# Performance work log

Hardware: AMD Instinct MI355X
Metric: run time of the kernel (lower is better)

## Reference

```python
import jax, jax.numpy as jnp
import numpy as np
from jax import lax

B, T = 64, 512
VOCAB, EMBED, UNITS = 32000, 256, 512


def setup_inputs() -> dict:
    key = jax.random.key(0)
    ks = jax.random.split(key, 8)
    s = 0.05
    G = 4 * UNITS
    return {
        "encoder_input": jax.random.randint(ks[0], (B, T), 0, VOCAB, dtype=jnp.int32),
        "embedding": jax.random.normal(ks[1], (VOCAB, EMBED), jnp.float32) * s,
        "W_fwd": jax.random.normal(ks[2], (EMBED, G), jnp.float32) * s,
        "U_fwd": jax.random.normal(ks[3], (UNITS, G), jnp.float32) * s,
        "b_fwd": jnp.zeros((G,), jnp.float32),
        "W_bwd": jax.random.normal(ks[4], (EMBED, G), jnp.float32) * s,
        "U_bwd": jax.random.normal(ks[5], (UNITS, G), jnp.float32) * s,
        "b_bwd": jnp.zeros((G,), jnp.float32),
    }


def _lstm_scan(x, mask, W, Uw, b, reverse):
    """Masked LSTM over time. Keras semantics: at masked steps the (h, c)
    state is carried through unchanged and the emitted output repeats the
    previous hidden state (which for LSTM equals the carried h).
    x: [B, T, E] float, mask: [B, T] bool."""
    Bsz = x.shape[0]
    Uh = Uw.shape[0]
    # Precompute input projection for all timesteps: [B, T, 4U]
    xz = jnp.einsum("bte,eg->btg", x, W) + b

    def step(carry, inp):
        h, c = carry
        z_x, m = inp  # z_x: [B, 4U], m: [B]
        z = z_x + h @ Uw
        i, f, g, o = jnp.split(z, 4, axis=-1)  # Keras gate order i, f, c, o
        i = jax.nn.sigmoid(i)
        f = jax.nn.sigmoid(f)
        g = jnp.tanh(g)
        o = jax.nn.sigmoid(o)
        c_new = f * c + i * g
        h_new = o * jnp.tanh(c_new)
        m = m[:, None]
        h = jnp.where(m, h_new, h)
        c = jnp.where(m, c_new, c)
        return (h, c), h

    h0 = jnp.zeros((Bsz, Uh), x.dtype)
    c0 = jnp.zeros((Bsz, Uh), x.dtype)
    (h, c), ys = lax.scan(
        step, (h0, c0), (xz.swapaxes(0, 1), mask.T), reverse=reverse
    )
    # lax.scan with reverse=True stacks outputs in original time order,
    # matching Keras Bidirectional's reverse-then-re-reverse behavior.
    return ys.swapaxes(0, 1), h, c


def reference(encoder_input, embedding, W_fwd, U_fwd, b_fwd, W_bwd, U_bwd, b_bwd):
    mask = encoder_input != 0  # mask_zero=True
    emb = embedding[encoder_input]  # [B, T, E]
    out_f, h_f, c_f = _lstm_scan(emb, mask, W_fwd, U_fwd, b_fwd, reverse=False)
    out_b, h_b, c_b = _lstm_scan(emb, mask, W_bwd, U_bwd, b_bwd, reverse=True)
    encoder_output = jnp.concatenate([out_f, out_b], axis=-1)  # [B, T, 2U]
    final_state_h = jnp.concatenate([h_f, h_b], axis=-1)  # [B, 2U]
    final_state_c = jnp.concatenate([c_f, c_b], axis=-1)  # [B, 2U]
    # Dropout is identity at inference (training=False default).
    return encoder_output, final_state_h, final_state_c
```

## Files before the change

### kernel.cpp

```cpp
#include <hip/hip_runtime.h>
#include <cstdint>


#define B_ 64
#define T_ 512
#define E_ 256

typedef __attribute__((ext_vector_type(8))) short bf16x8;
typedef __attribute__((ext_vector_type(4))) float f32x4;

__device__ __forceinline__ unsigned short f2bf(float x) {
  unsigned u = __float_as_uint(x);
  u += 0x7FFFu + ((u >> 16) & 1u);
  return (unsigned short)(u >> 16);
}
__device__ __forceinline__ float sigm(float x) { return 1.0f / (1.0f + __expf(-x)); }
__device__ __forceinline__ float tanh_(float x) { return 1.0f - 2.0f / (__expf(2.0f * x) + 1.0f); }

__global__ void prep_kernel(const int* __restrict__ enc, const float* __restrict__ emb,
                            unsigned short* __restrict__ o) {
  const int bi = blockIdx.x;
  const int t = bi >> 6, b = bi & 63;
  const int tok = enc[b * T_ + t];
  float4 v = ((const float4*)(emb + (size_t)tok * E_))[threadIdx.x];
  ushort4 w;
  w.x = f2bf(v.x); w.y = f2bf(v.y); w.z = f2bf(v.z); w.w = f2bf(v.w);
  ((ushort4*)(o + (size_t)t * (B_ * E_) + b * E_))[threadIdx.x] = w;
}

__global__ __launch_bounds__(256, 1)
void lstm_kernel(const int* __restrict__ enc, const unsigned short* __restrict__ embq,
                 const float* __restrict__ Wf, const float* __restrict__ Uf, const float* __restrict__ bfv,
                 const float* __restrict__ Wb, const float* __restrict__ Ub, const float* __restrict__ bbv,
                 unsigned short* __restrict__ Hbuf, unsigned* __restrict__ cnt,
                 float* __restrict__ out) {
  const int tid = threadIdx.x;
  const int lane = tid & 63;
  const int wave = tid >> 6;
  const int mh = wave & 1, nh = wave >> 1;
  const int l15 = lane & 15, l4 = lane >> 4;
  const int d = blockIdx.x >> 5;
  const int cg = blockIdx.x & 31;
  const int u0 = cg * 16;
  const float* Wd = d ? Wb : Wf;
  const float* Ud = d ? Ub : Uf;
  const float* bd = d ? bbv : bfv;

  __shared__ float Z[64][68];

  bf16x8 u_frag[16][2];
#pragma unroll
  for (int ks = 0; ks < 16; ++ks) {
#pragma unroll
    for (int ns = 0; ns < 2; ++ns) {
      const int gate = nh * 2 + ns;
      const int col = gate * 512 + u0 + l15;
      const int k0 = ks * 32 + l4 * 8;
      bf16x8 f;
#pragma unroll
      for (int i = 0; i < 8; ++i) f[i] = (short)f2bf(Ud[(size_t)(k0 + i) * 2048 + col]);
      u_frag[ks][ns] = f;
    }
  }
  bf16x8 w_frag[8][2];
#pragma unroll
  for (int ks = 0; ks < 8; ++ks) {
#pragma unroll
    for (int ns = 0; ns < 2; ++ns) {
      const int gate = nh * 2 + ns;
      const int col = gate * 512 + u0 + l15;
      const int k0 = ks * 32 + l4 * 8;
      bf16x8 f;
#pragma unroll
      for (int i = 0; i < 8; ++i) f[i] = (short)f2bf(Wd[(size_t)(k0 + i) * 2048 + col]);
      w_frag[ks][ns] = f;
    }
  }

  const int ej = tid & 15;
  const int ebg = tid >> 4;
  float bias[4];
#pragma unroll
  for (int g = 0; g < 4; ++g) bias[g] = bd[g * 512 + u0 + ej];

  float hst[4] = {0.f, 0.f, 0.f, 0.f}, cst[4] = {0.f, 0.f, 0.f, 0.f};

  bf16x8 apf[8][2];
  int mpf[4];
  {
    const int t0 = d ? 511 : 0;
    const unsigned short* eT = embq + (size_t)t0 * (B_ * E_);
#pragma unroll
    for (int ks = 0; ks < 8; ++ks)
#pragma unroll
      for (int ms = 0; ms < 2; ++ms) {
        const int b = mh * 32 + ms * 16 + l15;
        const int e0 = ks * 32 + l4 * 8;
        apf[ks][ms] = *(const bf16x8*)(eT + b * E_ + e0);
      }
#pragma unroll
    for (int r = 0; r < 4; ++r) mpf[r] = enc[(ebg * 4 + r) * T_ + t0];
  }

  unsigned* cntd = cnt + d * 513;

  for (int s = 0; s < 512; ++s) {
    const int t = d ? (511 - s) : s;
    f32x4 acc[2][2];
#pragma unroll
    for (int ms = 0; ms < 2; ++ms)
#pragma unroll
      for (int ns = 0; ns < 2; ++ns) acc[ms][ns] = (f32x4)0.0f;

#pragma unroll
    for (int ks = 0; ks < 8; ++ks)
#pragma unroll
      for (int ms = 0; ms < 2; ++ms)
#pragma unroll
        for (int ns = 0; ns < 2; ++ns)
          acc[ms][ns] = __builtin_amdgcn_mfma_f32_16x16x32_bf16(apf[ks][ms], w_frag[ks][ns],
                                                                acc[ms][ns], 0, 0, 0);

    if (s > 0) {
      if (tid == 0) {
        while (__hip_atomic_load(cntd + s, __ATOMIC_RELAXED, __HIP_MEMORY_SCOPE_AGENT) < 32u) {}
      }
      __syncthreads();

      bf16x8 ha[16][2];
      {
        const unsigned short* Hrd = Hbuf + ((size_t)((s & 1) * 2 + d)) * 32768;
        const char* lb = (const char*)Hrd + (l4 >> 1) * 2048 + mh * 1024 + l15 * 32 + (l4 & 1) * 16;
        const char* b0p = lb + 0 * 8192 + 4096;
        const char* b1p = lb + 1 * 8192 + 4096;
        const char* b2p = lb + 2 * 8192 + 4096;
        const char* b3p = lb + 3 * 8192 + 4096;
        const char* b4p = lb + 4 * 8192 + 4096;
        const char* b5p = lb + 5 * 8192 + 4096;
        const char* b6p = lb + 6 * 8192 + 4096;
        const char* b7p = lb + 7 * 8192 + 4096;
        asm volatile(
          "global_load_dwordx4 %0, %32, off offset:-4096 sc0 sc1\n\t"
          "global_load_dwordx4 %1, %32, off offset:-3584 sc0 sc1\n\t"
          "global_load_dwordx4 %2, %32, off offset:0 sc0 sc1\n\t"
          "global_load_dwordx4 %3, %32, off offset:512 sc0 sc1\n\t"
          "global_load_dwordx4 %4, %33, off offset:-4096 sc0 sc1\n\t"
          "global_load_dwordx4 %5, %33, off offset:-3584 sc0 sc1\n\t"
          "global_load_dwordx4 %6, %33, off offset:0 sc0 sc1\n\t"
          "global_load_dwordx4 %7, %33, off offset:512 sc0 sc1\n\t"
          "global_load_dwordx4 %8, %34, off offset:-4096 sc0 sc1\n\t"
          "global_load_dwordx4 %9, %34, off offset:-3584 sc0 sc1\n\t"
          "global_load_dwordx4 %10, %34, off offset:0 sc0 sc1\n\t"
          "global_load_dwordx4 %11, %34, off offset:512 sc0 sc1\n\t"
          "global_load_dwordx4 %12, %35, off offset:-4096 sc0 sc1\n\t"
          "global_load_dwordx4 %13, %35, off offset:-3584 sc0 sc1\n\t"
          "global_load_dwordx4 %14, %35, off offset:0 sc0 sc1\n\t"
          "global_load_dwordx4 %15, %35, off offset:512 sc0 sc1\n\t"
          "global_load_dwordx4 %16, %36, off offset:-4096 sc0 sc1\n\t"
          "global_load_dwordx4 %17, %36, off offset:-3584 sc0 sc1\n\t"
          "global_load_dwordx4 %18, %36, off offset:0 sc0 sc1\n\t"
          "global_load_dwordx4 %19, %36, off offset:512 sc0 sc1\n\t"
          "global_load_dwordx4 %20, %37, off offset:-4096 sc0 sc1\n\t"
          "global_load_dwordx4 %21, %37, off offset:-3584 sc0 sc1\n\t"
          "global_load_dwordx4 %22, %37, off offset:0 sc0 sc1\n\t"
          "global_load_dwordx4 %23, %37, off offset:512 sc0 sc1\n\t"
          "global_load_dwordx4 %24, %38, off offset:-4096 sc0 sc1\n\t"
          "global_load_dwordx4 %25, %38, off offset:-3584 sc0 sc1\n\t"
          "global_load_dwordx4 %26, %38, off offset:0 sc0 sc1\n\t"
          "global_load_dwordx4 %27, %38, off offset:512 sc0 sc1\n\t"
          "global_load_dwordx4 %28, %39, off offset:-4096 sc0 sc1\n\t"
          "global_load_dwordx4 %29, %39, off offset:-3584 sc0 sc1\n\t"
          "global_load_dwordx4 %30, %39, off offset:0 sc0 sc1\n\t"
          "global_load_dwordx4 %31, %39, off offset:512 sc0 sc1\n\t"
          "s_waitcnt vmcnt(0)"
          : "=v"(ha[0][0]), "=v"(ha[0][1]), "=v"(ha[1][0]), "=v"(ha[1][1]),
            "=v"(ha[2][0]), "=v"(ha[2][1]), "=v"(ha[3][0]), "=v"(ha[3][1]),
            "=v"(ha[4][0]), "=v"(ha[4][1]), "=v"(ha[5][0]), "=v"(ha[5][1]),
            "=v"(ha[6][0]), "=v"(ha[6][1]), "=v"(ha[7][0]), "=v"(ha[7][1]),
            "=v"(ha[8][0]), "=v"(ha[8][1]), "=v"(ha[9][0]), "=v"(ha[9][1]),
            "=v"(ha[10][0]), "=v"(ha[10][1]), "=v"(ha[11][0]), "=v"(ha[11][1]),
            "=v"(ha[12][0]), "=v"(ha[12][1]), "=v"(ha[13][0]), "=v"(ha[13][1]),
            "=v"(ha[14][0]), "=v"(ha[14][1]), "=v"(ha[15][0]), "=v"(ha[15][1])
          : "v"(b0p), "v"(b1p), "v"(b2p), "v"(b3p),
            "v"(b4p), "v"(b5p), "v"(b6p), "v"(b7p)
          : "memory");
      }
#pragma unroll
      for (int ks = 0; ks < 16; ++ks) {
        acc[0][0] = __builtin_amdgcn_mfma_f32_16x16x32_bf16(ha[ks][0], u_frag[ks][0], acc[0][0], 0, 0, 0);
        acc[0][1] = __builtin_amdgcn_mfma_f32_16x16x32_bf16(ha[ks][0], u_frag[ks][1], acc[0][1], 0, 0, 0);
        acc[1][0] = __builtin_amdgcn_mfma_f32_16x16x32_bf16(ha[ks][1], u_frag[ks][0], acc[1][0], 0, 0, 0);
        acc[1][1] = __builtin_amdgcn_mfma_f32_16x16x32_bf16(ha[ks][1], u_frag[ks][1], acc[1][1], 0, 0, 0);
      }
    } else {
      __syncthreads();
    }

#pragma unroll
    for (int ms = 0; ms < 2; ++ms)
#pragma unroll
      for (int ns = 0; ns < 2; ++ns)
#pragma unroll
        for (int r = 0; r < 4; ++r)
          Z[mh * 32 + ms * 16 + l4 * 4 + r][nh * 32 + ns * 16 + l15] = acc[ms][ns][r];
    __syncthreads();

    unsigned hu[4];
    {
      const bool last = (s == 511);
#pragma unroll
      for (int r = 0; r < 4; ++r) {
        const int b = ebg * 4 + r;
        float zi = Z[b][ej] + bias[0];
        float zf = Z[b][16 + ej] + bias[1];
        float zg = Z[b][32 + ej] + bias[2];
        float zo = Z[b][48 + ej] + bias[3];
        float ig = sigm(zi), fg = sigm(zf), gg = tanh_(zg), og = sigm(zo);
        float cn = fg * cst[r] + ig * gg;
        float hn = og * tanh_(cn);
        const bool m = (mpf[r] != 0);
        cst[r] = m ? cn : cst[r];
        hst[r] = m ? hn : hst[r];
        hu[r] = (unsigned)f2bf(hst[r]);
        out[((size_t)b * T_ + t) * 1024 + d * 512 + u0 + ej] = hst[r];
        if (last) {
          out[33554432u + (size_t)b * 1024 + d * 512 + u0 + ej] = hst[r];
          out[33619968u + (size_t)b * 1024 + d * 512 + u0 + ej] = cst[r];
        }
      }
    }

    if (s < 511) {
      const int tn = d ? (510 - s) : (s + 1);
      const unsigned short* eT = embq + (size_t)tn * (B_ * E_);
#pragma unroll
      for (int ks = 0; ks < 8; ++ks)
#pragma unroll
        for (int ms = 0; ms < 2; ++ms) {
          const int b = mh * 32 + ms * 16 + l15;
          const int e0 = ks * 32 + l4 * 8;
          apf[ks][ms] = *(const bf16x8*)(eT + b * E_ + e0);
        }
#pragma unroll
      for (int r = 0; r < 4; ++r) mpf[r] = enc[(ebg * 4 + r) * T_ + tn];
    }

    {
      unsigned short* Hwr = Hbuf + ((size_t)(((s + 1) & 1) * 2 + d)) * 32768 + cg * 1024;
      char* hp = (char*)(Hwr + ebg * 64 + ej);
      asm volatile(
        "global_store_short %0, %1, off sc0 sc1\n\t"
        "global_store_short %0, %2, off offset:32 sc0 sc1\n\t"
        "global_store_short %0, %3, off offset:64 sc0 sc1\n\t"
        "global_store_short %0, %4, off offset:96 sc0 sc1\n\t"
        "s_waitcnt vmcnt(0)"
        :: "v"(hp), "v"(hu[0]), "v"(hu[1]), "v"(hu[2]), "v"(hu[3])
        : "memory");
    }
    __syncthreads();
    if (tid == 0)
      __hip_atomic_fetch_add(cntd + (s + 1), 1u, __ATOMIC_RELAXED, __HIP_MEMORY_SCOPE_AGENT);
  }
}

extern "C" void kernel_launch(void* const* d_in, const int* in_sizes, int n_in,
                              void* d_out, int out_size, void* d_ws, size_t ws_size,
                              hipStream_t stream) {
  const int* enc = (const int*)d_in[0];
  const float* emb = (const float*)d_in[1];
  const float* Wf = (const float*)d_in[2];
  const float* Uf = (const float*)d_in[3];
  const float* bf = (const float*)d_in[4];
  const float* Wb = (const float*)d_in[5];
  const float* Ub = (const float*)d_in[6];
  const float* bb = (const float*)d_in[7];
  float* out = (float*)d_out;
  char* ws = (char*)d_ws;

  unsigned short* embq = (unsigned short*)ws;
  unsigned short* Hbuf = (unsigned short*)(ws + (16u << 20));
  unsigned* cnt = (unsigned*)(ws + (16u << 20) + 262144u);

  hipMemsetAsync(ws + (16u << 20) + 262144u, 0, 4104u, stream);
  prep_kernel<<<32768, 64, 0, stream>>>(enc, emb, embq);
  lstm_kernel<<<64, 256, 0, stream>>>(enc, embq, Wf, Uf, bf, Wb, Ub, bb, Hbuf, cnt, out);
}
```

Measured before the change: 3.415 ms.

## Replace persistent spin-synced LSTM kernel with per-timestep kernel launches

```diff
diff --git a/kernel.cpp b/kernel.cpp
--- a/kernel.cpp
+++ b/kernel.cpp
@@ -28,12 +28,37 @@
   ((ushort4*)(o + (size_t)t * (B_ * E_) + b * E_))[threadIdx.x] = w;
 }
 
+__global__ void prep_w(const float* __restrict__ Wf, const float* __restrict__ Uf,
+                       const float* __restrict__ Wb, const float* __restrict__ Ub,
+                       unsigned short* __restrict__ Uq, unsigned short* __restrict__ Wq) {
+  int bi = blockIdx.x;
+  const int ns = bi & 1; bi >>= 1;
+  const int kk = bi % 24; bi /= 24;
+  const int nh = bi & 1; bi >>= 1;
+  const int cg = bi & 31; bi >>= 5;
+  const int d = bi;
+  const int lane = threadIdx.x;
+  const int l15 = lane & 15, l4 = lane >> 4;
+  const bool isU = (kk < 16);
+  const float* src = isU ? (d ? Ub : Uf) : (d ? Wb : Wf);
+  const int ks = isU ? kk : (kk - 16);
+  const int col = (nh * 2 + ns) * 512 + cg * 16 + l15;
+  const int row0 = ks * 32 + l4 * 8;
+  bf16x8 f;
+#pragma unroll
+  for (int i = 0; i < 8; ++i) f[i] = (short)f2bf(src[(size_t)(row0 + i) * 2048 + col]);
+  unsigned short* dst = isU
+    ? Uq + ((size_t)(((d * 32 + cg) * 2 + nh) * 16 + ks) * 2 + ns) * 512 + lane * 8
+    : Wq + ((size_t)(((d * 32 + cg) * 2 + nh) * 8 + ks) * 2 + ns) * 512 + lane * 8;
+  *(bf16x8*)dst = f;
+}
+
 __global__ __launch_bounds__(256, 1)
-void lstm_kernel(const int* __restrict__ enc, const unsigned short* __restrict__ embq,
-                 const float* __restrict__ Wf, const float* __restrict__ Uf, const float* __restrict__ bfv,
-                 const float* __restrict__ Wb, const float* __restrict__ Ub, const float* __restrict__ bbv,
-                 unsigned short* __restrict__ Hbuf, unsigned* __restrict__ cnt,
-                 float* __restrict__ out) {
+void lstm_step(const int s, const int* __restrict__ enc, const unsigned short* __restrict__ embq,
+               const unsigned short* __restrict__ Uq, const unsigned short* __restrict__ Wq,
+               const float* __restrict__ bfv, const float* __restrict__ bbv,
+               unsigned short* __restrict__ Hbf, float* __restrict__ Hf32,
+               float* __restrict__ Cst, float* __restrict__ out) {
   const int tid = threadIdx.x;
   const int lane = tid & 63;
   const int wave = tid >> 6;
@@ -42,224 +67,117 @@
   const int d = blockIdx.x >> 5;
   const int cg = blockIdx.x & 31;
   const int u0 = cg * 16;
-  const float* Wd = d ? Wb : Wf;
-  const float* Ud = d ? Ub : Uf;
-  const float* bd = d ? bbv : bfv;
+  const int t = d ? (T_ - 1 - s) : s;
 
   __shared__ float Z[64][68];
 
+  const unsigned short* ub = Uq + ((size_t)((d * 32 + cg) * 2 + nh)) * (16 * 2 * 512);
+  const unsigned short* wb = Wq + ((size_t)((d * 32 + cg) * 2 + nh)) * (8 * 2 * 512);
   bf16x8 u_frag[16][2];
 #pragma unroll
-  for (int ks = 0; ks < 16; ++ks) {
-#pragma unroll
-    for (int ns = 0; ns < 2; ++ns) {
-      const int gate = nh * 2 + ns;
-      const int col = gate * 512 + u0 + l15;
-      const int k0 = ks * 32 + l4 * 8;
-      bf16x8 f;
-#pragma unroll
-      for (int i = 0; i < 8; ++i) f[i] = (short)f2bf(Ud[(size_t)(k0 + i) * 2048 + col]);
-      u_frag[ks][ns] = f;
+  for (int ks = 0; ks < 16; ++ks)
+#pragma unroll
+    for (int ns = 0; ns < 2; ++ns)
+      u_frag[ks][ns] = *(const bf16x8*)(ub + (size_t)(ks * 2 + ns) * 512 + lane * 8);
+  bf16x8 w_frag[8][2];
+#pragma unroll
+  for (int ks = 0; ks < 8; ++ks)
+#pragma unroll
+    for (int ns = 0; ns < 2; ++ns)
+      w_frag[ks][ns] = *(const bf16x8*)(wb + (size_t)(ks * 2 + ns) * 512 + lane * 8);
+
+  bf16x8 apf[8][2];
+  {
+    const unsigned short* eT = embq + (size_t)t * (B_ * E_);
+#pragma unroll
+    for (int ks = 0; ks < 8; ++ks)
+#pragma unroll
+      for (int ms = 0; ms < 2; ++ms) {
+        const int b = mh * 32 + ms * 16 + l15;
+        apf[ks][ms] = *(const bf16x8*)(eT + b * E_ + ks * 32 + l4 * 8);
+      }
+  }
+  const int ej = tid & 15;
+  const int ebg = tid >> 4;
+  int mpf[4];
+#pragma unroll
+  for (int r = 0; r < 4; ++r) mpf[r] = enc[(ebg * 4 + r) * T_ + t];
+
+  f32x4 acc[2][2];
+#pragma unroll
+  for (int ms = 0; ms < 2; ++ms)
+#pragma unroll
+    for (int ns = 0; ns < 2; ++ns) acc[ms][ns] = (f32x4)0.0f;
+
+#pragma unroll
+  for (int ks = 0; ks < 8; ++ks)
+#pragma unroll
+    for (int ms = 0; ms < 2; ++ms)
+#pragma unroll
+      for (int ns = 0; ns < 2; ++ns)
+        acc[ms][ns] = __builtin_amdgcn_mfma_f32_16x16x32_bf16(apf[ks][ms], w_frag[ks][ns],
+                                                              acc[ms][ns], 0, 0, 0);
+
+  if (s > 0) {
+    const unsigned short* Hrd = Hbf + ((size_t)((s & 1) * 2 + d)) * (B_ * 512);
+    bf16x8 ha[16][2];
+#pragma unroll
+    for (int ks = 0; ks < 16; ++ks)
+#pragma unroll
+      for (int ms = 0; ms < 2; ++ms) {
+        const int b = mh * 32 + ms * 16 + l15;
+        ha[ks][ms] = *(const bf16x8*)(Hrd + (size_t)b * 512 + ks * 32 + l4 * 8);
+      }
+#pragma unroll
+    for (int ks = 0; ks < 16; ++ks) {
+      acc[0][0] = __builtin_amdgcn_mfma_f32_16x16x32_bf16(ha[ks][0], u_frag[ks][0], acc[0][0], 0, 0, 0);
+      acc[0][1] = __builtin_amdgcn_mfma_f32_16x16x32_bf16(ha[ks][0], u_frag[ks][1], acc[0][1], 0, 0, 0);
+      acc[1][0] = __builtin_amdgcn_mfma_f32_16x16x32_bf16(ha[ks][1], u_frag[ks][0], acc[1][0], 0, 0, 0);
+      acc[1][1] = __builtin_amdgcn_mfma_f32_16x16x32_bf16(ha[ks][1], u_frag[ks][1], acc[1][1], 0, 0, 0);
     }
   }
-  bf16x8 w_frag[8][2];
-#pragma unroll
-  for (int ks = 0; ks < 8; ++ks) {
-#pragma unroll
-    for (int ns = 0; ns < 2; ++ns) {
-      const int gate = nh * 2 + ns;
-      const int col = gate * 512 + u0 + l15;
-      const int k0 = ks * 32 + l4 * 8;
-      bf16x8 f;
-#pragma unroll
-      for (int i = 0; i < 8; ++i) f[i] = (short)f2bf(Wd[(size_t)(k0 + i) * 2048 + col]);
-      w_frag[ks][ns] = f;
+
+#pragma unroll
+  for (int ms = 0; ms < 2; ++ms)
+#pragma unroll
+    for (int ns = 0; ns < 2; ++ns)
+#pragma unroll
+      for (int r = 0; r < 4; ++r)
+        Z[mh * 32 + ms * 16 + l4 * 4 + r][nh * 32 + ns * 16 + l15] = acc[ms][ns][r];
+  __syncthreads();
+
+  const float* bd = d ? bbv : bfv;
+  float bias[4];
+#pragma unroll
+  for (int g = 0; g < 4; ++g) bias[g] = bd[g * 512 + u0 + ej];
+
+  float* Hf = Hf32 + (size_t)d * (B_ * 512);
+  float* Cf = Cst + (size_t)d * (B_ * 512);
+  unsigned short* Hwr = Hbf + ((size_t)(((s + 1) & 1) * 2 + d)) * (B_ * 512);
+  const bool last = (s == T_ - 1);
+#pragma unroll
+  for (int r = 0; r < 4; ++r) {
+    const int b = ebg * 4 + r;
+    const size_t si = (size_t)b * 512 + u0 + ej;
+    float zi = Z[b][ej] + bias[0];
+    float zf = Z[b][16 + ej] + bias[1];
+    float zg = Z[b][32 + ej] + bias[2];
+    float zo = Z[b][48 + ej] + bias[3];
+    float ig = sigm(zi), fg = sigm(zf), gg = tanh_(zg), og = sigm(zo);
+    float hp = Hf[si], cp = Cf[si];
+    float cn = fg * cp + ig * gg;
+    float hn = og * tanh_(cn);
+    const bool m = (mpf[r] != 0);
+    float hv = m ? hn : hp;
+    float cv = m ? cn : cp;
+    Hf[si] = hv;
+    Cf[si] = cv;
+    Hwr[si] = f2bf(hv);
+    out[((size_t)b * T_ + t) * 1024 + d * 512 + u0 + ej] = hv;
+    if (last) {
+      out[33554432u + (size_t)b * 1024 + d * 512 + u0 + ej] = hv;
+      out[33619968u + (size_t)b * 1024 + d * 512 + u0 + ej] = cv;
     }
-  }
-
-  const int ej = tid & 15;
-  const int ebg = tid >> 4;
-  float bias[4];
-#pragma unroll
-  for (int g = 0; g < 4; ++g) bias[g] = bd[g * 512 + u0 + ej];
-
-  float hst[4] = {0.f, 0.f, 0.f, 0.f}, cst[4] = {0.f, 0.f, 0.f, 0.f};
-
-  bf16x8 apf[8][2];
-  int mpf[4];
-  {
-    const int t0 = d ? 511 : 0;
-    const unsigned short* eT = embq + (size_t)t0 * (B_ * E_);
-#pragma unroll
-    for (int ks = 0; ks < 8; ++ks)
-#pragma unroll
-      for (int ms = 0; ms < 2; ++ms) {
-        const int b = mh * 32 + ms * 16 + l15;
-        const int e0 = ks * 32 + l4 * 8;
-        apf[ks][ms] = *(const bf16x8*)(eT + b * E_ + e0);
-      }
-#pragma unroll
-    for (int r = 0; r < 4; ++r) mpf[r] = enc[(ebg * 4 + r) * T_ + t0];
-  }
-
-  unsigned* cntd = cnt + d * 513;
-
-  for (int s = 0; s < 512; ++s) {
-    const int t = d ? (511 - s) : s;
-    f32x4 acc[2][2];
-#pragma unroll
-    for (int ms = 0; ms < 2; ++ms)
-#pragma unroll
-      for (int ns = 0; ns < 2; ++ns) acc[ms][ns] = (f32x4)0.0f;
-
-#pragma unroll
-    for (int ks = 0; ks < 8; ++ks)
-#pragma unroll
-      for (int ms = 0; ms < 2; ++ms)
-#pragma unroll
-        for (int ns = 0; ns < 2; ++ns)
-          acc[ms][ns] = __builtin_amdgcn_mfma_f32_16x16x32_bf16(apf[ks][ms], w_frag[ks][ns],
-                                                                acc[ms][ns], 0, 0, 0);
-
-    if (s > 0) {
-      if (tid == 0) {
-        while (__hip_atomic_load(cntd + s, __ATOMIC_RELAXED, __HIP_MEMORY_SCOPE_AGENT) < 32u) {}
-      }
-      __syncthreads();
-
-      bf16x8 ha[16][2];
-      {
-        const unsigned short* Hrd = Hbuf + ((size_t)((s & 1) * 2 + d)) * 32768;
-        const char* lb = (const char*)Hrd + (l4 >> 1) * 2048 + mh * 1024 + l15 * 32 + (l4 & 1) * 16;
-        const char* b0p = lb + 0 * 8192 + 4096;
-        const char* b1p = lb + 1 * 8192 + 4096;
-        const char* b2p = lb + 2 * 8192 + 4096;
-        const char* b3p = lb + 3 * 8192 + 4096;
-        const char* b4p = lb + 4 * 8192 + 4096;
-        const char* b5p = lb + 5 * 8192 + 4096;
-        const char* b6p = lb + 6 * 8192 + 4096;
-        const char* b7p = lb + 7 * 8192 + 4096;
-        asm volatile(
-          "global_load_dwordx4 %0, %32, off offset:-4096 sc0 sc1\n\t"
-          "global_load_dwordx4 %1, %32, off offset:-3584 sc0 sc1\n\t"
-          "global_load_dwordx4 %2, %32, off offset:0 sc0 sc1\n\t"
-          "global_load_dwordx4 %3, %32, off offset:512 sc0 sc1\n\t"
-          "global_load_dwordx4 %4, %33, off offset:-4096 sc0 sc1\n\t"
-          "global_load_dwordx4 %5, %33, off offset:-3584 sc0 sc1\n\t"
-          "global_load_dwordx4 %6, %33, off offset:0 sc0 sc1\n\t"
-          "global_load_dwordx4 %7, %33, off offset:512 sc0 sc1\n\t"
-          "global_load_dwordx4 %8, %34, off offset:-4096 sc0 sc1\n\t"
-          "global_load_dwordx4 %9, %34, off offset:-3584 sc0 sc1\n\t"
-          "global_load_dwordx4 %10, %34, off offset:0 sc0 sc1\n\t"
-          "global_load_dwordx4 %11, %34, off offset:512 sc0 sc1\n\t"
-          "global_load_dwordx4 %12, %35, off offset:-4096 sc0 sc1\n\t"
-          "global_load_dwordx4 %13, %35, off offset:-3584 sc0 sc1\n\t"
-          "global_load_dwordx4 %14, %35, off offset:0 sc0 sc1\n\t"
-          "global_load_dwordx4 %15, %35, off offset:512 sc0 sc1\n\t"
-          "global_load_dwordx4 %16, %36, off offset:-4096 sc0 sc1\n\t"
-          "global_load_dwordx4 %17, %36, off offset:-3584 sc0 sc1\n\t"
-          "global_load_dwordx4 %18, %36, off offset:0 sc0 sc1\n\t"
-          "global_load_dwordx4 %19, %36, off offset:512 sc0 sc1\n\t"
-          "global_load_dwordx4 %20, %37, off offset:-4096 sc0 sc1\n\t"
-          "global_load_dwordx4 %21, %37, off offset:-3584 sc0 sc1\n\t"
-          "global_load_dwordx4 %22, %37, off offset:0 sc0 sc1\n\t"
-          "global_load_dwordx4 %23, %37, off offset:512 sc0 sc1\n\t"
-          "global_load_dwordx4 %24, %38, off offset:-4096 sc0 sc1\n\t"
-          "global_load_dwordx4 %25, %38, off offset:-3584 sc0 sc1\n\t"
-          "global_load_dwordx4 %26, %38, off offset:0 sc0 sc1\n\t"
-          "global_load_dwordx4 %27, %38, off offset:512 sc0 sc1\n\t"
-          "global_load_dwordx4 %28, %39, off offset:-4096 sc0 sc1\n\t"
-          "global_load_dwordx4 %29, %39, off offset:-3584 sc0 sc1\n\t"
-          "global_load_dwordx4 %30, %39, off offset:0 sc0 sc1\n\t"
-          "global_load_dwordx4 %31, %39, off offset:512 sc0 sc1\n\t"
-          "s_waitcnt vmcnt(0)"
-          : "=v"(ha[0][0]), "=v"(ha[0][1]), "=v"(ha[1][0]), "=v"(ha[1][1]),
-            "=v"(ha[2][0]), "=v"(ha[2][1]), "=v"(ha[3][0]), "=v"(ha[3][1]),
-            "=v"(ha[4][0]), "=v"(ha[4][1]), "=v"(ha[5][0]), "=v"(ha[5][1]),
-            "=v"(ha[6][0]), "=v"(ha[6][1]), "=v"(ha[7][0]), "=v"(ha[7][1]),
-            "=v"(ha[8][0]), "=v"(ha[8][1]), "=v"(ha[9][0]), "=v"(ha[9][1]),
-            "=v"(ha[10][0]), "=v"(ha[10][1]), "=v"(ha[11][0]), "=v"(ha[11][1]),
-            "=v"(ha[12][0]), "=v"(ha[12][1]), "=v"(ha[13][0]), "=v"(ha[13][1]),
-            "=v"(ha[14][0]), "=v"(ha[14][1]), "=v"(ha[15][0]), "=v"(ha[15][1])
-          : "v"(b0p), "v"(b1p), "v"(b2p), "v"(b3p),
-            "v"(b4p), "v"(b5p), "v"(b6p), "v"(b7p)
-          : "memory");
-      }
-#pragma unroll
-      for (int ks = 0; ks < 16; ++ks) {
-        acc[0][0] = __builtin_amdgcn_mfma_f32_16x16x32_bf16(ha[ks][0], u_frag[ks][0], acc[0][0], 0, 0, 0);
-        acc[0][1] = __builtin_amdgcn_mfma_f32_16x16x32_bf16(ha[ks][0], u_frag[ks][1], acc[0][1], 0, 0, 0);
-        acc[1][0] = __builtin_amdgcn_mfma_f32_16x16x32_bf16(ha[ks][1], u_frag[ks][0], acc[1][0], 0, 0, 0);
-        acc[1][1] = __builtin_amdgcn_mfma_f32_16x16x32_bf16(ha[ks][1], u_frag[ks][1], acc[1][1], 0, 0, 0);
-      }
-    } else {
-      __syncthreads();
-    }
-
-#pragma unroll
-    for (int ms = 0; ms < 2; ++ms)
-#pragma unroll
-      for (int ns = 0; ns < 2; ++ns)
-#pragma unroll
-        for (int r = 0; r < 4; ++r)
-          Z[mh * 32 + ms * 16 + l4 * 4 + r][nh * 32 + ns * 16 + l15] = acc[ms][ns][r];
-    __syncthreads();
-
-    unsigned hu[4];
-    {
-      const bool last = (s == 511);
-#pragma unroll
-      for (int r = 0; r < 4; ++r) {
-        const int b = ebg * 4 + r;
-        float zi = Z[b][ej] + bias[0];
-        float zf = Z[b][16 + ej] + bias[1];
-        float zg = Z[b][32 + ej] + bias[2];
-        float zo = Z[b][48 + ej] + bias[3];
-        float ig = sigm(zi), fg = sigm(zf), gg = tanh_(zg), og = sigm(zo);
-        float cn = fg * cst[r] + ig * gg;
-        float hn = og * tanh_(cn);
-        const bool m = (mpf[r] != 0);
-        cst[r] = m ? cn : cst[r];
-        hst[r] = m ? hn : hst[r];
-        hu[r] = (unsigned)f2bf(hst[r]);
-        out[((size_t)b * T_ + t) * 1024 + d * 512 + u0 + ej] = hst[r];
-        if (last) {
-          out[33554432u + (size_t)b * 1024 + d * 512 + u0 + ej] = hst[r];
-          out[33619968u + (size_t)b * 1024 + d * 512 + u0 + ej] = cst[r];
-        }
-      }
-    }
-
-    if (s < 511) {
-      const int tn = d ? (510 - s) : (s + 1);
-      const unsigned short* eT = embq + (size_t)tn * (B_ * E_);
-#pragma unroll
-      for (int ks = 0; ks < 8; ++ks)
-#pragma unroll
-        for (int ms = 0; ms < 2; ++ms) {
-          const int b = mh * 32 + ms * 16 + l15;
-          const int e0 = ks * 32 + l4 * 8;
-          apf[ks][ms] = *(const bf16x8*)(eT + b * E_ + e0);
-        }
-#pragma unroll
-      for (int r = 0; r < 4; ++r) mpf[r] = enc[(ebg * 4 + r) * T_ + tn];
-    }
-
-    {
-      unsigned short* Hwr = Hbuf + ((size_t)(((s + 1) & 1) * 2 + d)) * 32768 + cg * 1024;
-      char* hp = (char*)(Hwr + ebg * 64 + ej);
-      asm volatile(
-        "global_store_short %0, %1, off sc0 sc1\n\t"
-        "global_store_short %0, %2, off offset:32 sc0 sc1\n\t"
-        "global_store_short %0, %3, off offset:64 sc0 sc1\n\t"
-        "global_store_short %0, %4, off offset:96 sc0 sc1\n\t"
-        "s_waitcnt vmcnt(0)"
-        :: "v"(hp), "v"(hu[0]), "v"(hu[1]), "v"(hu[2]), "v"(hu[3])
-        : "memory");
-    }
-    __syncthreads();
-    if (tid == 0)
-      __hip_atomic_fetch_add(cntd + (s + 1), 1u, __ATOMIC_RELAXED, __HIP_MEMORY_SCOPE_AGENT);
   }
 }
 
@@ -278,10 +196,15 @@
   char* ws = (char*)d_ws;
 
   unsigned short* embq = (unsigned short*)ws;
-  unsigned short* Hbuf = (unsigned short*)(ws + (16u << 20));
-  unsigned* cnt = (unsigned*)(ws + (16u << 20) + 262144u);
-
-  hipMemsetAsync(ws + (16u << 20) + 262144u, 0, 4104u, stream);
+  unsigned short* Uq  = (unsigned short*)(ws + 16777216u);
+  unsigned short* Wq  = (unsigned short*)(ws + 20971520u);
+  unsigned short* Hbf = (unsigned short*)(ws + 23068672u);
+  float* Hf32 = (float*)(ws + 23330816u);
+  float* Cst  = (float*)(ws + 23592960u);
+
+  hipMemsetAsync(ws + 23068672u, 0, 786432u, stream);
   prep_kernel<<<32768, 64, 0, stream>>>(enc, emb, embq);
-  lstm_kernel<<<64, 256, 0, stream>>>(enc, embq, Wf, Uf, bf, Wb, Ub, bb, Hbuf, cnt, out);
-}
+  prep_w<<<6144, 64, 0, stream>>>(Wf, Uf, Wb, Ub, Uq, Wq);
+  for (int s = 0; s < 512; ++s)
+    lstm_step<<<64, 256, 0, stream>>>(s, enc, embq, Uq, Wq, bf, bb, Hbf, Hf32, Cst, out);
+}
```

Measured after the change: 7.037 ms. 2.06x slower.
